# Performance work log

Measured on AMD Instinct MI355X. Metric: run time of the kernel, lower is better.

The kernel has to match this reference:

```python
import jax, jax.numpy as jnp
import numpy as np

S = 2048      # sequence length (q_seq == kv_seq, self-attention)
D = 1024      # hidden_size
H = 16        # num_heads
DH = D // H   # per-head dim
LN_EPS = 1e-5


def setup_inputs() -> dict:
    key = jax.random.key(0)
    ks = jax.random.split(key, 8)
    init = lambda k, shape: (jax.random.normal(k, shape, dtype=jnp.float32)
                             / np.float32(np.sqrt(shape[-1])))
    return {
        "x": jax.random.normal(ks[0], (S, D), dtype=jnp.float32),
        "logit_bias": jax.random.normal(ks[1], (S, H * S), dtype=jnp.float32) * 0.1,
        "mask": jax.random.bernoulli(ks[2], 0.9, (S, S)),
        "Wq": init(ks[3], (D, D)),
        "Wk": init(ks[4], (D, D)),
        "Wv": init(ks[5], (D, D)),
        "Wo": init(ks[6], (D, D)),
        "ln_w": jnp.ones((D,), dtype=jnp.float32),
        "ln_b": jnp.zeros((D,), dtype=jnp.float32),
    }


def reference(x, logit_bias, mask, Wq, Wk, Wv, Wo, ln_w, ln_b):
    # Projections (eqx.nn.Linear: y = W @ x, no bias), split into heads.
    q = (x @ Wq.T).reshape(S, H, DH)  # [s,h,d]
    k = (x @ Wk.T).reshape(S, H, DH)  # [S,h,d]
    v = (x @ Wv.T).reshape(S, H, DH)  # [S,h,d]

    # Scaled scores + per-head additive logit bias.
    scale = jnp.asarray(1.0 / np.sqrt(DH), dtype=q.dtype)
    logits = jnp.einsum('shd,Shd->hsS', q * scale, k)  # [h,s,S]
    logits = logits + logit_bias.reshape(S, H, S).transpose(1, 0, 2)

    # Boolean mask (q_seq, kv_seq) broadcast over heads.
    logits = jnp.where(mask[None, :, :], logits, jnp.finfo(logits.dtype).min)

    # Stable softmax in float32 (matches result_type promotion in source).
    weights = jax.nn.softmax(logits.astype(jnp.float32), axis=-1).astype(logits.dtype)

    attn = jnp.einsum('hsS,Shd->shd', weights, v).reshape(S, D)
    attn_out = attn @ Wo.T  # output projection, no bias

    # Residual + LayerNorm over last dim (eqx.nn.LayerNorm, eps=1e-5).
    res = attn_out + x
    mean = jnp.mean(res, axis=-1, keepdims=True)
    var = jnp.var(res, axis=-1, keepdims=True)
    normed = (res - mean) * jax.lax.rsqrt(var + LN_EPS)
    return normed * ln_w + ln_b
```

## Files before the change

kernel.cpp:

```cpp
#include <hip/hip_runtime.h>

#define SS 2048
#define DD 1024
#define HH 16
#define DHD 64
#define HSN (HH * SS)

typedef __bf16 bf16x8 __attribute__((ext_vector_type(8)));
typedef __bf16 bf16x4 __attribute__((ext_vector_type(4)));
typedef float f32x4 __attribute__((ext_vector_type(4)));

__global__ __launch_bounds__(256) void cvt_bf16_kernel(const float* __restrict__ in,
                                                       __bf16* __restrict__ out, int n4) {
  int i = blockIdx.x * 256 + threadIdx.x;
  if (i >= n4) return;
  const float4 v = ((const float4*)in)[i];
  bf16x4 r;
  r[0] = (__bf16)v.x; r[1] = (__bf16)v.y; r[2] = (__bf16)v.z; r[3] = (__bf16)v.w;
  *(bf16x4*)&out[(long)i * 4] = r;
}

template <int MODE>
__global__ __launch_bounds__(256) void gemm_nt(const __bf16* __restrict__ A,
                                               const __bf16* __restrict__ B,
                                               void* __restrict__ Cout,
                                               int M, int N, int K) {
  __shared__ __bf16 As[64][40];
  __shared__ __bf16 Bs[64][40];
  const int tid = threadIdx.x;
  const int lane = tid & 63;
  const int wave = tid >> 6;
  const int wm = (wave >> 1) * 32;
  const int wn = (wave & 1) * 32;
  const long m0 = (long)blockIdx.y * 64;
  const long n0 = (long)blockIdx.x * 64;
  const int g = lane >> 4;
  const int r16 = lane & 15;
  const int lrow = tid >> 2;
  const int lseg = (tid & 3) * 8;

  f32x4 acc[2][2] = {};

  for (int k0 = 0; k0 < K; k0 += 32) {
    *(bf16x8*)&As[lrow][lseg] = *(const bf16x8*)&A[(m0 + lrow) * K + k0 + lseg];
    *(bf16x8*)&Bs[lrow][lseg] = *(const bf16x8*)&B[(n0 + lrow) * K + k0 + lseg];
    __syncthreads();
    bf16x8 af[2], bfr[2];
#pragma unroll
    for (int r = 0; r < 2; ++r) af[r] = *(const bf16x8*)&As[wm + r * 16 + r16][g * 8];
#pragma unroll
    for (int c = 0; c < 2; ++c) bfr[c] = *(const bf16x8*)&Bs[wn + c * 16 + r16][g * 8];
#pragma unroll
    for (int r = 0; r < 2; ++r)
#pragma unroll
      for (int c = 0; c < 2; ++c)
        acc[r][c] = __builtin_amdgcn_mfma_f32_16x16x32_bf16(af[r], bfr[c], acc[r][c], 0, 0, 0);
    __syncthreads();
  }

#pragma unroll
  for (int r = 0; r < 2; ++r)
#pragma unroll
    for (int c = 0; c < 2; ++c)
#pragma unroll
      for (int i = 0; i < 4; ++i) {
        const long row = m0 + wm + r * 16 + g * 4 + i;
        const long col = n0 + wn + c * 16 + r16;
        float v = acc[r][c][i];
        if (MODE == 1) v *= 0.125f;
        if (MODE == 2) ((float*)Cout)[row * N + col] = v;
        else           ((__bf16*)Cout)[row * N + col] = (__bf16)v;
      }
}

__global__ __launch_bounds__(256) void transpose_bf16(const __bf16* __restrict__ in,
                                                      __bf16* __restrict__ out,
                                                      int R, int C) {
  __shared__ __bf16 t[64][72];
  const int tid = threadIdx.x;
  const long r0 = (long)blockIdx.y * 64;
  const long c0 = (long)blockIdx.x * 64;
  const int row = tid >> 2;
#pragma unroll
  for (int it = 0; it < 2; ++it) {
    const int seg = (tid & 3) * 8 + it * 32;
    *(bf16x8*)&t[row][seg] = *(const bf16x8*)&in[(r0 + row) * C + c0 + seg];
  }
  __syncthreads();
#pragma unroll
  for (int it = 0; it < 2; ++it) {
    const int seg = (tid & 3) * 8 + it * 32;
    bf16x8 v;
#pragma unroll
    for (int j = 0; j < 8; ++j) v[j] = t[seg + j][row];
    *(bf16x8*)&out[(c0 + row) * R + r0 + seg] = v;
  }
}

__global__ __launch_bounds__(256) void attn_kernel(
    const __bf16* __restrict__ Q, const __bf16* __restrict__ K,
    const __bf16* __restrict__ Vt, const float* __restrict__ bias,
    const int* __restrict__ mask, __bf16* __restrict__ Aout) {
  __shared__ __bf16 Ks[32][72];
  __shared__ __bf16 Vts[64][40];
  __shared__ __bf16 Ps[4][16][40];
  const int tid = threadIdx.x;
  const int lane = tid & 63;
  const int wave = tid >> 6;
  const int h = blockIdx.y;
  const int q0 = blockIdx.x * 64 + wave * 16;
  const int g = lane >> 4;
  const int r16 = lane & 15;

  bf16x8 qf[2];
#pragma unroll
  for (int m = 0; m < 2; ++m)
    qf[m] = *(const bf16x8*)&Q[(long)(q0 + r16) * DD + h * DHD + m * 32 + g * 8];

  f32x4 o[4] = {};
  float mrow[4], lsum[4];
#pragma unroll
  for (int i = 0; i < 4; ++i) { mrow[i] = -__builtin_inff(); lsum[i] = 0.f; }

  const int krow = tid >> 3, kseg = (tid & 7) * 8;
  const int vrow = tid >> 2, vseg = (tid & 3) * 8;

  for (int kv0 = 0; kv0 < SS; kv0 += 32) {
    *(bf16x8*)&Ks[krow][kseg]  = *(const bf16x8*)&K[(long)(kv0 + krow) * DD + h * DHD + kseg];
    *(bf16x8*)&Vts[vrow][vseg] = *(const bf16x8*)&Vt[(long)(h * DHD + vrow) * SS + kv0 + vseg];
    __syncthreads();

#pragma unroll
    for (int t = 0; t < 2; ++t) {
      bf16x8 kf0 = *(const bf16x8*)&Ks[t * 16 + r16][g * 8];
      bf16x8 kf1 = *(const bf16x8*)&Ks[t * 16 + r16][32 + g * 8];
      f32x4 s = {};
      s = __builtin_amdgcn_mfma_f32_16x16x32_bf16(qf[0], kf0, s, 0, 0, 0);
      s = __builtin_amdgcn_mfma_f32_16x16x32_bf16(qf[1], kf1, s, 0, 0, 0);
      const int kcol = kv0 + t * 16 + r16;
#pragma unroll
      for (int i = 0; i < 4; ++i) {
        const int qrow = q0 + g * 4 + i;
        float sv = s[i] + bias[(long)qrow * HSN + h * SS + kcol];
        if (mask[(long)qrow * SS + kcol] == 0) sv = -3.4028235e38f;
        float tmax = sv;
        tmax = fmaxf(tmax, __shfl_xor(tmax, 1));
        tmax = fmaxf(tmax, __shfl_xor(tmax, 2));
        tmax = fmaxf(tmax, __shfl_xor(tmax, 4));
        tmax = fmaxf(tmax, __shfl_xor(tmax, 8));
        const float mnew = fmaxf(mrow[i], tmax);
        const float alpha = __expf(mrow[i] - mnew);
        const float p = __expf(sv - mnew);
        float psum = p;
        psum += __shfl_xor(psum, 1);
        psum += __shfl_xor(psum, 2);
        psum += __shfl_xor(psum, 4);
        psum += __shfl_xor(psum, 8);
        lsum[i] = lsum[i] * alpha + psum;
        mrow[i] = mnew;
#pragma unroll
        for (int db = 0; db < 4; ++db) o[db][i] *= alpha;
        Ps[wave][g * 4 + i][t * 16 + r16] = (__bf16)p;
      }
    }

    bf16x8 pf = *(const bf16x8*)&Ps[wave][r16][g * 8];
#pragma unroll
    for (int db = 0; db < 4; ++db) {
      bf16x8 vf = *(const bf16x8*)&Vts[db * 16 + r16][g * 8];
      o[db] = __builtin_amdgcn_mfma_f32_16x16x32_bf16(pf, vf, o[db], 0, 0, 0);
    }
    __syncthreads();
  }

#pragma unroll
  for (int db = 0; db < 4; ++db)
#pragma unroll
    for (int i = 0; i < 4; ++i) {
      const int row = q0 + g * 4 + i;
      Aout[(long)row * DD + h * DHD + db * 16 + r16] = (__bf16)(o[db][i] / lsum[i]);
    }
}

__global__ __launch_bounds__(256) void ln_kernel(const float* __restrict__ attn_out,
                                                 const float* __restrict__ x,
                                                 const float* __restrict__ w,
                                                 const float* __restrict__ b,
                                                 float* __restrict__ out) {
  const long row = blockIdx.x;
  const int tid = threadIdx.x;
  float v[4];
  float s = 0.f, s2 = 0.f;
#pragma unroll
  for (int j = 0; j < 4; ++j) {
    const int d = tid + j * 256;
    const float r = attn_out[row * DD + d] + x[row * DD + d];
    v[j] = r; s += r; s2 += r * r;
  }
#pragma unroll
  for (int off = 1; off < 64; off <<= 1) {
    s  += __shfl_xor(s, off);
    s2 += __shfl_xor(s2, off);
  }
  __shared__ float ss[4], ss2[4];
  if ((tid & 63) == 0) { ss[tid >> 6] = s; ss2[tid >> 6] = s2; }
  __syncthreads();
  s = ss[0] + ss[1] + ss[2] + ss[3];
  s2 = ss2[0] + ss2[1] + ss2[2] + ss2[3];
  const float mean = s * (1.f / DD);
  const float var = s2 * (1.f / DD) - mean * mean;
  const float inv = rsqrtf(var + 1e-5f);
#pragma unroll
  for (int j = 0; j < 4; ++j) {
    const int d = tid + j * 256;
    out[row * DD + d] = (v[j] - mean) * inv * w[d] + b[d];
  }
}

extern "C" void kernel_launch(void* const* d_in, const int* in_sizes, int n_in,
                              void* d_out, int out_size, void* d_ws, size_t ws_size,
                              hipStream_t stream) {
  const float* x    = (const float*)d_in[0];
  const float* bias = (const float*)d_in[1];
  const int*   mask = (const int*)d_in[2];
  const float* Wq   = (const float*)d_in[3];
  const float* Wk   = (const float*)d_in[4];
  const float* Wv   = (const float*)d_in[5];
  const float* Wo   = (const float*)d_in[6];
  const float* lnw  = (const float*)d_in[7];
  const float* lnb  = (const float*)d_in[8];
  float* out = (float*)d_out;

  char* ws = (char*)d_ws;
  const size_t MB = 1024 * 1024;
  __bf16* xb   = (__bf16*)(ws + 0);
  __bf16* Wqb  = (__bf16*)(ws + 4 * MB);
  __bf16* Wkb  = (__bf16*)(ws + 6 * MB);
  __bf16* Wvb  = (__bf16*)(ws + 8 * MB);
  __bf16* Wob  = (__bf16*)(ws + 10 * MB);
  __bf16* Qb   = (__bf16*)(ws + 12 * MB);
  __bf16* Kb   = (__bf16*)(ws + 16 * MB);
  __bf16* Vb   = (__bf16*)(ws + 20 * MB);
  __bf16* Vtb  = (__bf16*)(ws + 24 * MB);
  __bf16* Atnb = (__bf16*)(ws + 28 * MB);
  float*  AOut = (float*)(ws + 32 * MB);

  cvt_bf16_kernel<<<dim3(SS * DD / 1024), dim3(256), 0, stream>>>(x, xb, SS * DD / 4);
  cvt_bf16_kernel<<<dim3(DD * DD / 1024), dim3(256), 0, stream>>>(Wq, Wqb, DD * DD / 4);
  cvt_bf16_kernel<<<dim3(DD * DD / 1024), dim3(256), 0, stream>>>(Wk, Wkb, DD * DD / 4);
  cvt_bf16_kernel<<<dim3(DD * DD / 1024), dim3(256), 0, stream>>>(Wv, Wvb, DD * DD / 4);
  cvt_bf16_kernel<<<dim3(DD * DD / 1024), dim3(256), 0, stream>>>(Wo, Wob, DD * DD / 4);

  dim3 ggrid(DD / 64, SS / 64);
  gemm_nt<1><<<ggrid, dim3(256), 0, stream>>>(xb, Wqb, Qb, SS, DD, DD);
  gemm_nt<0><<<ggrid, dim3(256), 0, stream>>>(xb, Wkb, Kb, SS, DD, DD);
  gemm_nt<0><<<ggrid, dim3(256), 0, stream>>>(xb, Wvb, Vb, SS, DD, DD);

  transpose_bf16<<<dim3(DD / 64, SS / 64), dim3(256), 0, stream>>>(Vb, Vtb, SS, DD);

  attn_kernel<<<dim3(SS / 64, HH), dim3(256), 0, stream>>>(Qb, Kb, Vtb, bias, mask, Atnb);

  gemm_nt<2><<<ggrid, dim3(256), 0, stream>>>(Atnb, Wob, AOut, SS, DD, DD);

  ln_kernel<<<dim3(SS), dim3(256), 0, stream>>>(AOut, x, lnw, lnb, out);
}
```

Measured before the change: 576.0 us.

## Split-KV attention with combine, 128-tile fused QKV GEMM using direct-to-LDS loads

The three Q/K/V projections become one launch using 128x128 tiles and global_load_lds copies, and the output GEMM uses the same body. Attention now processes 64-key tiles and works in base 2, with the softmax scale times log2e folded into Q. It is split across up to 4 KV partitions written as fp32 partial outputs plus row max and sum, then merged by a new combine kernel. This raises parallelism and cuts per-tile softmax and sync overhead, at the cost of extra partial-output memory traffic and one more launch.

```diff
diff --git a/kernel.cpp b/kernel.cpp
--- a/kernel.cpp
+++ b/kernel.cpp
@@ -5,10 +5,18 @@
 #define HH 16
 #define DHD 64
 #define HSN (HH * SS)
+#define LOG2E 1.44269504088896340736f
 
 typedef __bf16 bf16x8 __attribute__((ext_vector_type(8)));
 typedef __bf16 bf16x4 __attribute__((ext_vector_type(4)));
 typedef float f32x4 __attribute__((ext_vector_type(4)));
+typedef unsigned int u32;
+
+__device__ __forceinline__ void glds16(const void* g, void* l) {
+  __builtin_amdgcn_global_load_lds(
+      (const __attribute__((address_space(1))) u32*)(const u32*)g,
+      (__attribute__((address_space(3))) u32*)(u32*)l, 16, 0, 0);
+}
 
 __global__ __launch_bounds__(256) void cvt_bf16_kernel(const float* __restrict__ in,
                                                        __bf16* __restrict__ out, int n4) {
@@ -20,57 +28,74 @@
   *(bf16x4*)&out[(long)i * 4] = r;
 }
 
-template <int MODE>
-__global__ __launch_bounds__(256) void gemm_nt(const __bf16* __restrict__ A,
-                                               const __bf16* __restrict__ B,
-                                               void* __restrict__ Cout,
-                                               int M, int N, int K) {
-  __shared__ __bf16 As[64][40];
-  __shared__ __bf16 Bs[64][40];
+template <int OUTF32>
+__device__ __forceinline__ void gemm128_body(const __bf16* __restrict__ A,
+                                             const __bf16* __restrict__ B,
+                                             void* __restrict__ Cout, float scale) {
+  __shared__ alignas(16) __bf16 As[128 * 32];
+  __shared__ alignas(16) __bf16 Bs[128 * 32];
   const int tid = threadIdx.x;
   const int lane = tid & 63;
   const int wave = tid >> 6;
-  const int wm = (wave >> 1) * 32;
-  const int wn = (wave & 1) * 32;
-  const long m0 = (long)blockIdx.y * 64;
-  const long n0 = (long)blockIdx.x * 64;
-  const int g = lane >> 4;
-  const int r16 = lane & 15;
-  const int lrow = tid >> 2;
-  const int lseg = (tid & 3) * 8;
-
-  f32x4 acc[2][2] = {};
-
-  for (int k0 = 0; k0 < K; k0 += 32) {
-    *(bf16x8*)&As[lrow][lseg] = *(const bf16x8*)&A[(m0 + lrow) * K + k0 + lseg];
-    *(bf16x8*)&Bs[lrow][lseg] = *(const bf16x8*)&B[(n0 + lrow) * K + k0 + lseg];
+  const long m0 = (long)blockIdx.y * 128;
+  const long n0 = (long)blockIdx.x * 128;
+  const int wm = (wave >> 1) * 64;
+  const int wn = (wave & 1) * 64;
+  const int g = lane >> 4, r16 = lane & 15;
+  const int srow = tid >> 2, sseg = (tid & 3) * 8;
+
+  f32x4 acc[4][4] = {};
+
+  for (int k0 = 0; k0 < DD; k0 += 32) {
+#pragma unroll
+    for (int it = 0; it < 2; ++it) {
+      const int row = srow + it * 64;
+      glds16(&A[(m0 + row) * DD + k0 + sseg], &As[row * 32 + sseg]);
+      glds16(&B[(n0 + row) * DD + k0 + sseg], &Bs[row * 32 + sseg]);
+    }
     __syncthreads();
-    bf16x8 af[2], bfr[2];
-#pragma unroll
-    for (int r = 0; r < 2; ++r) af[r] = *(const bf16x8*)&As[wm + r * 16 + r16][g * 8];
-#pragma unroll
-    for (int c = 0; c < 2; ++c) bfr[c] = *(const bf16x8*)&Bs[wn + c * 16 + r16][g * 8];
-#pragma unroll
-    for (int r = 0; r < 2; ++r)
-#pragma unroll
-      for (int c = 0; c < 2; ++c)
+    bf16x8 af[4], bfr[4];
+#pragma unroll
+    for (int r = 0; r < 4; ++r) af[r] = *(const bf16x8*)&As[(wm + r * 16 + r16) * 32 + g * 8];
+#pragma unroll
+    for (int c = 0; c < 4; ++c) bfr[c] = *(const bf16x8*)&Bs[(wn + c * 16 + r16) * 32 + g * 8];
+#pragma unroll
+    for (int r = 0; r < 4; ++r)
+#pragma unroll
+      for (int c = 0; c < 4; ++c)
         acc[r][c] = __builtin_amdgcn_mfma_f32_16x16x32_bf16(af[r], bfr[c], acc[r][c], 0, 0, 0);
     __syncthreads();
   }
 
 #pragma unroll
-  for (int r = 0; r < 2; ++r)
-#pragma unroll
-    for (int c = 0; c < 2; ++c)
+  for (int r = 0; r < 4; ++r)
+#pragma unroll
+    for (int c = 0; c < 4; ++c)
 #pragma unroll
       for (int i = 0; i < 4; ++i) {
         const long row = m0 + wm + r * 16 + g * 4 + i;
         const long col = n0 + wn + c * 16 + r16;
-        float v = acc[r][c][i];
-        if (MODE == 1) v *= 0.125f;
-        if (MODE == 2) ((float*)Cout)[row * N + col] = v;
-        else           ((__bf16*)Cout)[row * N + col] = (__bf16)v;
+        const float v = acc[r][c][i] * scale;
+        if (OUTF32) ((float*)Cout)[row * DD + col] = v;
+        else        ((__bf16*)Cout)[row * DD + col] = (__bf16)v;
       }
+}
+
+__global__ __launch_bounds__(256) void gemm_qkv(const __bf16* __restrict__ A,
+                                                const __bf16* __restrict__ B0,
+                                                const __bf16* __restrict__ B1,
+                                                const __bf16* __restrict__ B2,
+                                                __bf16* C0, __bf16* C1, __bf16* C2,
+                                                float s0) {
+  const __bf16* B = blockIdx.z == 0 ? B0 : (blockIdx.z == 1 ? B1 : B2);
+  __bf16* C = blockIdx.z == 0 ? C0 : (blockIdx.z == 1 ? C1 : C2);
+  gemm128_body<0>(A, B, C, blockIdx.z == 0 ? s0 : 1.0f);
+}
+
+__global__ __launch_bounds__(256) void gemm_o(const __bf16* __restrict__ A,
+                                              const __bf16* __restrict__ B,
+                                              float* __restrict__ C) {
+  gemm128_body<1>(A, B, C, 1.0f);
 }
 
 __global__ __launch_bounds__(256) void transpose_bf16(const __bf16* __restrict__ in,
@@ -100,17 +125,20 @@
 __global__ __launch_bounds__(256) void attn_kernel(
     const __bf16* __restrict__ Q, const __bf16* __restrict__ K,
     const __bf16* __restrict__ Vt, const float* __restrict__ bias,
-    const int* __restrict__ mask, __bf16* __restrict__ Aout) {
-  __shared__ __bf16 Ks[32][72];
-  __shared__ __bf16 Vts[64][40];
-  __shared__ __bf16 Ps[4][16][40];
+    const int* __restrict__ mask, float* __restrict__ Opart,
+    float* __restrict__ Mpart, float* __restrict__ Lpart) {
+  __shared__ alignas(16) __bf16 Ks[64][72];
+  __shared__ alignas(16) __bf16 Vts[64][72];
+  __shared__ alignas(16) __bf16 Ps[4][16][72];
   const int tid = threadIdx.x;
   const int lane = tid & 63;
   const int wave = tid >> 6;
   const int h = blockIdx.y;
+  const int z = blockIdx.z;
   const int q0 = blockIdx.x * 64 + wave * 16;
-  const int g = lane >> 4;
-  const int r16 = lane & 15;
+  const int g = lane >> 4, r16 = lane & 15;
+  const int kvlen = SS / gridDim.z;
+  const int kvbeg = z * kvlen;
 
   bf16x8 qf[2];
 #pragma unroll
@@ -122,64 +150,119 @@
 #pragma unroll
   for (int i = 0; i < 4; ++i) { mrow[i] = -__builtin_inff(); lsum[i] = 0.f; }
 
-  const int krow = tid >> 3, kseg = (tid & 7) * 8;
-  const int vrow = tid >> 2, vseg = (tid & 3) * 8;
-
-  for (int kv0 = 0; kv0 < SS; kv0 += 32) {
-    *(bf16x8*)&Ks[krow][kseg]  = *(const bf16x8*)&K[(long)(kv0 + krow) * DD + h * DHD + kseg];
-    *(bf16x8*)&Vts[vrow][vseg] = *(const bf16x8*)&Vt[(long)(h * DHD + vrow) * SS + kv0 + vseg];
+  const int srow = tid >> 2;
+
+  for (int kv0 = kvbeg; kv0 < kvbeg + kvlen; kv0 += 64) {
     __syncthreads();
-
-#pragma unroll
-    for (int t = 0; t < 2; ++t) {
+#pragma unroll
+    for (int it = 0; it < 2; ++it) {
+      const int seg = (tid & 3) + it * 4;
+      *(bf16x8*)&Ks[srow][seg * 8] =
+          *(const bf16x8*)&K[(long)(kv0 + srow) * DD + h * DHD + seg * 8];
+      *(bf16x8*)&Vts[srow][seg * 8] =
+          *(const bf16x8*)&Vt[(long)(h * DHD + srow) * SS + kv0 + seg * 8];
+    }
+    __syncthreads();
+
+    f32x4 s[4];
+#pragma unroll
+    for (int t = 0; t < 4; ++t) {
       bf16x8 kf0 = *(const bf16x8*)&Ks[t * 16 + r16][g * 8];
       bf16x8 kf1 = *(const bf16x8*)&Ks[t * 16 + r16][32 + g * 8];
-      f32x4 s = {};
-      s = __builtin_amdgcn_mfma_f32_16x16x32_bf16(qf[0], kf0, s, 0, 0, 0);
-      s = __builtin_amdgcn_mfma_f32_16x16x32_bf16(qf[1], kf1, s, 0, 0, 0);
+      f32x4 acc = {};
+      acc = __builtin_amdgcn_mfma_f32_16x16x32_bf16(qf[0], kf0, acc, 0, 0, 0);
+      s[t] = __builtin_amdgcn_mfma_f32_16x16x32_bf16(qf[1], kf1, acc, 0, 0, 0);
+    }
+
+    float sv[4][4];
+#pragma unroll
+    for (int t = 0; t < 4; ++t) {
       const int kcol = kv0 + t * 16 + r16;
 #pragma unroll
       for (int i = 0; i < 4; ++i) {
         const int qrow = q0 + g * 4 + i;
-        float sv = s[i] + bias[(long)qrow * HSN + h * SS + kcol];
-        if (mask[(long)qrow * SS + kcol] == 0) sv = -3.4028235e38f;
-        float tmax = sv;
-        tmax = fmaxf(tmax, __shfl_xor(tmax, 1));
-        tmax = fmaxf(tmax, __shfl_xor(tmax, 2));
-        tmax = fmaxf(tmax, __shfl_xor(tmax, 4));
-        tmax = fmaxf(tmax, __shfl_xor(tmax, 8));
-        const float mnew = fmaxf(mrow[i], tmax);
-        const float alpha = __expf(mrow[i] - mnew);
-        const float p = __expf(sv - mnew);
-        float psum = p;
-        psum += __shfl_xor(psum, 1);
-        psum += __shfl_xor(psum, 2);
-        psum += __shfl_xor(psum, 4);
-        psum += __shfl_xor(psum, 8);
-        lsum[i] = lsum[i] * alpha + psum;
-        mrow[i] = mnew;
-#pragma unroll
-        for (int db = 0; db < 4; ++db) o[db][i] *= alpha;
-        Ps[wave][g * 4 + i][t * 16 + r16] = (__bf16)p;
+        const float bv = bias[(long)qrow * HSN + h * SS + kcol];
+        const int mv = mask[(long)qrow * SS + kcol];
+        sv[t][i] = mv ? s[t][i] + bv * LOG2E : -1e38f;
       }
     }
 
-    bf16x8 pf = *(const bf16x8*)&Ps[wave][r16][g * 8];
-#pragma unroll
-    for (int db = 0; db < 4; ++db) {
-      bf16x8 vf = *(const bf16x8*)&Vts[db * 16 + r16][g * 8];
-      o[db] = __builtin_amdgcn_mfma_f32_16x16x32_bf16(pf, vf, o[db], 0, 0, 0);
-    }
-    __syncthreads();
+#pragma unroll
+    for (int i = 0; i < 4; ++i) {
+      float m4 = fmaxf(fmaxf(sv[0][i], sv[1][i]), fmaxf(sv[2][i], sv[3][i]));
+      m4 = fmaxf(m4, __shfl_xor(m4, 1));
+      m4 = fmaxf(m4, __shfl_xor(m4, 2));
+      m4 = fmaxf(m4, __shfl_xor(m4, 4));
+      m4 = fmaxf(m4, __shfl_xor(m4, 8));
+      const float mnew = fmaxf(mrow[i], m4);
+      const float alpha = exp2f(mrow[i] - mnew);
+      const float p0 = exp2f(sv[0][i] - mnew);
+      const float p1 = exp2f(sv[1][i] - mnew);
+      const float p2 = exp2f(sv[2][i] - mnew);
+      const float p3 = exp2f(sv[3][i] - mnew);
+      float ps = (p0 + p1) + (p2 + p3);
+      ps += __shfl_xor(ps, 1);
+      ps += __shfl_xor(ps, 2);
+      ps += __shfl_xor(ps, 4);
+      ps += __shfl_xor(ps, 8);
+      lsum[i] = lsum[i] * alpha + ps;
+      mrow[i] = mnew;
+#pragma unroll
+      for (int db = 0; db < 4; ++db) o[db][i] *= alpha;
+      Ps[wave][g * 4 + i][r16]      = (__bf16)p0;
+      Ps[wave][g * 4 + i][16 + r16] = (__bf16)p1;
+      Ps[wave][g * 4 + i][32 + r16] = (__bf16)p2;
+      Ps[wave][g * 4 + i][48 + r16] = (__bf16)p3;
+    }
+
+#pragma unroll
+    for (int kh = 0; kh < 2; ++kh) {
+      bf16x8 pf = *(const bf16x8*)&Ps[wave][r16][kh * 32 + g * 8];
+#pragma unroll
+      for (int db = 0; db < 4; ++db) {
+        bf16x8 vf = *(const bf16x8*)&Vts[db * 16 + r16][kh * 32 + g * 8];
+        o[db] = __builtin_amdgcn_mfma_f32_16x16x32_bf16(pf, vf, o[db], 0, 0, 0);
+      }
+    }
   }
 
 #pragma unroll
   for (int db = 0; db < 4; ++db)
 #pragma unroll
     for (int i = 0; i < 4; ++i) {
-      const int row = q0 + g * 4 + i;
-      Aout[(long)row * DD + h * DHD + db * 16 + r16] = (__bf16)(o[db][i] / lsum[i]);
-    }
+      const long row = q0 + g * 4 + i;
+      Opart[((long)z * SS + row) * DD + h * DHD + db * 16 + r16] = o[db][i];
+    }
+  if (r16 == 0) {
+#pragma unroll
+    for (int i = 0; i < 4; ++i) {
+      const long row = q0 + g * 4 + i;
+      Mpart[((long)z * SS + row) * HH + h] = mrow[i];
+      Lpart[((long)z * SS + row) * HH + h] = lsum[i];
+    }
+  }
+}
+
+__global__ __launch_bounds__(256) void attn_combine(const float* __restrict__ Opart,
+                                                    const float* __restrict__ Mpart,
+                                                    const float* __restrict__ Lpart,
+                                                    __bf16* __restrict__ Aout, int nsplit) {
+  const int q = blockIdx.y;
+  const int idx = blockIdx.x * 256 + threadIdx.x;
+  const int h = idx >> 6;
+  float M = -__builtin_inff();
+  float mz[8];
+  for (int zz = 0; zz < nsplit; ++zz) {
+    mz[zz] = Mpart[((long)zz * SS + q) * HH + h];
+    M = fmaxf(M, mz[zz]);
+  }
+  float num = 0.f, den = 0.f;
+  for (int zz = 0; zz < nsplit; ++zz) {
+    const float w = exp2f(mz[zz] - M);
+    num += w * Opart[((long)zz * SS + q) * DD + idx];
+    den += w * Lpart[((long)zz * SS + q) * HH + h];
+  }
+  Aout[(long)q * DD + idx] = (__bf16)(num / den);
 }
 
 __global__ __launch_bounds__(256) void ln_kernel(const float* __restrict__ attn_out,
@@ -244,6 +327,15 @@
   __bf16* Vtb  = (__bf16*)(ws + 24 * MB);
   __bf16* Atnb = (__bf16*)(ws + 28 * MB);
   float*  AOut = (float*)(ws + 32 * MB);
+  const size_t base = 40 * MB;
+
+  int nsplit = 4;
+  while (nsplit > 1 &&
+         base + (size_t)nsplit * (8 * MB + 2 * (size_t)SS * HH * 4) > ws_size)
+    nsplit >>= 1;
+  float* Opart = (float*)(ws + base);
+  float* Mpart = (float*)(ws + base + (size_t)nsplit * 8 * MB);
+  float* Lpart = Mpart + (size_t)nsplit * SS * HH;
 
   cvt_bf16_kernel<<<dim3(SS * DD / 1024), dim3(256), 0, stream>>>(x, xb, SS * DD / 4);
   cvt_bf16_kernel<<<dim3(DD * DD / 1024), dim3(256), 0, stream>>>(Wq, Wqb, DD * DD / 4);
@@ -251,16 +343,16 @@
   cvt_bf16_kernel<<<dim3(DD * DD / 1024), dim3(256), 0, stream>>>(Wv, Wvb, DD * DD / 4);
   cvt_bf16_kernel<<<dim3(DD * DD / 1024), dim3(256), 0, stream>>>(Wo, Wob, DD * DD / 4);
 
-  dim3 ggrid(DD / 64, SS / 64);
-  gemm_nt<1><<<ggrid, dim3(256), 0, stream>>>(xb, Wqb, Qb, SS, DD, DD);
-  gemm_nt<0><<<ggrid, dim3(256), 0, stream>>>(xb, Wkb, Kb, SS, DD, DD);
-  gemm_nt<0><<<ggrid, dim3(256), 0, stream>>>(xb, Wvb, Vb, SS, DD, DD);
+  gemm_qkv<<<dim3(DD / 128, SS / 128, 3), dim3(256), 0, stream>>>(
+      xb, Wqb, Wkb, Wvb, Qb, Kb, Vb, 0.125f * LOG2E);
 
   transpose_bf16<<<dim3(DD / 64, SS / 64), dim3(256), 0, stream>>>(Vb, Vtb, SS, DD);
 
-  attn_kernel<<<dim3(SS / 64, HH), dim3(256), 0, stream>>>(Qb, Kb, Vtb, bias, mask, Atnb);
-
-  gemm_nt<2><<<ggrid, dim3(256), 0, stream>>>(Atnb, Wob, AOut, SS, DD, DD);
+  attn_kernel<<<dim3(SS / 64, HH, nsplit), dim3(256), 0, stream>>>(
+      Qb, Kb, Vtb, bias, mask, Opart, Mpart, Lpart);
+  attn_combine<<<dim3(DD / 256, SS), dim3(256), 0, stream>>>(Opart, Mpart, Lpart, Atnb, nsplit);
+
+  gemm_o<<<dim3(DD / 128, SS / 128), dim3(256), 0, stream>>>(Atnb, Wob, AOut);
 
   ln_kernel<<<dim3(SS), dim3(256), 0, stream>>>(AOut, x, lnw, lnb, out);
 }
```

Result: slower. 713.7 us (+23.9%).
